# Kernel tuning notes

Measured on AMD Instinct MI355X. Metric: run time of the kernel, lower is better.

The kernel has to match this reference:

```python
import jax, jax.numpy as jnp
import numpy as np

D_M = 1024
VOCAB = 50257
BASE = 10000.0
B, S = 8, 4096


def setup_inputs() -> dict:
    key = jax.random.key(0)
    k1, k2 = jax.random.split(key)
    x = jax.random.randint(k1, (B, S), 0, VOCAB, dtype=jnp.int64)
    emb_table = jax.random.normal(k2, (VOCAB, D_M), dtype=jnp.float32)
    return {"x": x, "emb_table": emb_table}


def _positional_encoding(seq_len, d_m, base, dtype):
    # Vectorized version of the original Python loop over d_m/2:
    # denoms[:, i] = arange(seq_len) / base**(2*i/d_m); even cols sin, odd cols cos.
    pos = jnp.arange(seq_len, dtype=dtype)                    # [S]
    i = jnp.arange(d_m // 2, dtype=dtype)                     # [D/2]
    inv_freq = jnp.power(jnp.asarray(base, dtype), -2.0 * i / d_m)  # [D/2]
    ang = pos[:, None] * inv_freq[None, :]                    # [S, D/2]
    pe = jnp.stack([jnp.sin(ang), jnp.cos(ang)], axis=-1)     # [S, D/2, 2]
    return pe.reshape(seq_len, d_m)                           # interleaved sin/cos


def reference(x, emb_table):
    # Embedding gather: [B, S] -> [B, S, D]
    emb = emb_table[x]
    pe = _positional_encoding(x.shape[1], emb_table.shape[1], BASE, emb_table.dtype)
    return emb + pe[None, :, :]
```

## Files before the change

kernel.cpp:

```cpp
#include <hip/hip_runtime.h>
#include <math.h>


#define D_M 1024
#define SEQ 4096

__global__ __launch_bounds__(256) void SinusoidalEmbedding_83030307766274_kernel(
    const int* __restrict__ x,
    const float* __restrict__ emb_table,
    float* __restrict__ out)
{
    const int t  = blockIdx.x;
    const int d4 = threadIdx.x;
    const int s  = t & (SEQ - 1);

    const int row = x[t];
    const float4* __restrict__ src = (const float4*)(emb_table + (size_t)row * D_M);
    float4 v = src[d4];

    const float c = -2.0f * 13.28771237954945f / (float)D_M;
    const float i0 = (float)(2 * d4);
    const float f0 = exp2f(i0 * c);
    const float f1 = exp2f((i0 + 1.0f) * c);
    const float sp = (float)s;

    float s0, c0, s1, c1;
    sincosf(sp * f0, &s0, &c0);
    sincosf(sp * f1, &s1, &c1);

    v.x += s0;
    v.y += c0;
    v.z += s1;
    v.w += c1;

    ((float4*)out)[(size_t)t * (D_M / 4) + d4] = v;
}

extern "C" void kernel_launch(void* const* d_in, const int* in_sizes, int n_in,
                              void* d_out, int out_size, void* d_ws, size_t ws_size,
                              hipStream_t stream)
{
    const int*   x         = (const int*)d_in[0];
    const float* emb_table = (const float*)d_in[1];
    float*       out       = (float*)d_out;

    const int n_tokens = in_sizes[0];
    SinusoidalEmbedding_83030307766274_kernel<<<n_tokens, 256, 0, stream>>>(x, emb_table, out);
}
```

Before: 301.2 us.

## Reuse sinusoidal encoding across batch by processing all batches per sequence block

Each block now handles one sequence position for all 8 batch rows. It computes the sin/cos positional terms once and applies them to 8 gathered embedding rows, with all 8 loads issued up front so more memory requests are in flight. This removes redundant transcendental math and raises memory-level parallelism. In exchange the grid shrinks from 32768 to 4096 blocks, register use per thread goes up, and the batch size is hardcoded to 8 instead of being read from the input size.

```diff
diff --git a/kernel.cpp b/kernel.cpp
--- a/kernel.cpp
+++ b/kernel.cpp
@@ -2,23 +2,32 @@
 #include <math.h>
 
 
-#define D_M 1024
-#define SEQ 4096
+#define D_M  1024
+#define SEQ  4096
+#define NB   8
 
 __global__ __launch_bounds__(256) void SinusoidalEmbedding_83030307766274_kernel(
     const int* __restrict__ x,
     const float* __restrict__ emb_table,
     float* __restrict__ out)
 {
-    const int t  = blockIdx.x;
+    const int s  = blockIdx.x;
     const int d4 = threadIdx.x;
-    const int s  = t & (SEQ - 1);
 
-    const int row = x[t];
-    const float4* __restrict__ src = (const float4*)(emb_table + (size_t)row * D_M);
-    float4 v = src[d4];
+    int rows[NB];
+#pragma unroll
+    for (int b = 0; b < NB; ++b)
+        rows[b] = x[b * SEQ + s];
 
-    const float c = -2.0f * 13.28771237954945f / (float)D_M;
+    float4 v[NB];
+#pragma unroll
+    for (int b = 0; b < NB; ++b) {
+        const float4* __restrict__ src =
+            (const float4*)(emb_table + (size_t)rows[b] * D_M);
+        v[b] = src[d4];
+    }
+
+    const float c  = -2.0f * 13.28771237954945f / (float)D_M;
     const float i0 = (float)(2 * d4);
     const float f0 = exp2f(i0 * c);
     const float f1 = exp2f((i0 + 1.0f) * c);
@@ -28,12 +37,16 @@
     sincosf(sp * f0, &s0, &c0);
     sincosf(sp * f1, &s1, &c1);
 
-    v.x += s0;
-    v.y += c0;
-    v.z += s1;
-    v.w += c1;
-
-    ((float4*)out)[(size_t)t * (D_M / 4) + d4] = v;
+    const size_t out_d4 = (size_t)d4;
+#pragma unroll
+    for (int b = 0; b < NB; ++b) {
+        float4 o = v[b];
+        o.x += s0;
+        o.y += c0;
+        o.z += s1;
+        o.w += c1;
+        ((float4*)out)[((size_t)b * SEQ + s) * (D_M / 4) + out_d4] = o;
+    }
 }
 
 extern "C" void kernel_launch(void* const* d_in, const int* in_sizes, int n_in,
@@ -44,6 +57,5 @@
     const float* emb_table = (const float*)d_in[1];
     float*       out       = (float*)d_out;
 
-    const int n_tokens = in_sizes[0];
-    SinusoidalEmbedding_83030307766274_kernel<<<n_tokens, 256, 0, stream>>>(x, emb_table, out);
+    SinusoidalEmbedding_83030307766274_kernel<<<SEQ, 256, 0, stream>>>(x, emb_table, out);
 }
```

Result: no change. 306.7 us (+1.8%).
